# Kernel tuning notes

Measured on AMD Instinct MI355X. Metric: run time of the kernel, lower is better.

The kernel has to match this reference:

```python
import jax, jax.numpy as jnp
import numpy as np

DIM = 256
RADIUS = 3
DIAM = 2 * RADIUS + 1          # 7
NNEIGH = DIAM * DIAM           # 49
B, H, W = 2, 64, 64
EPS_LN = 1e-6
EPS_NORM = 1e-7


def conv1x1(x, w, b):
    # x: [B,Cin,H,W], w: [Cout,Cin], b: [Cout]
    return jnp.einsum('oi,bihw->bohw', w, x) + b[None, :, None, None]


def layernorm2d(x, g, b):
    # channel-wise norm as in LayerNorm2d (mean/var over channel dim)
    u = x.mean(1, keepdims=True)
    s = ((x - u) ** 2).mean(1, keepdims=True)
    xn = (x - u) / jnp.sqrt(s + EPS_LN)
    return g[None, :, None, None] * xn + b[None, :, None, None]


def unfold_reflect(x, r):
    # torch F.unfold(pad(x, reflect, r), kernel=2r+1).reshape(B,C,D*D,H,W)
    d = 2 * r + 1
    hh, ww = x.shape[2], x.shape[3]
    xp = jnp.pad(x, ((0, 0), (0, 0), (r, r), (r, r)), mode='reflect')
    pats = [xp[:, :, i:i + hh, j:j + ww] for i in range(d) for j in range(d)]
    return jnp.stack(pats, axis=2)  # [B,C,D*D,H,W]


def setup_inputs() -> dict:
    key = jax.random.key(0)
    ks = jax.random.split(key, 20)
    sc_c = 1.0 / np.sqrt(DIM)
    sc_f = 1.0 / np.sqrt(NNEIGH + DIM)
    inp = {
        'spatial_feats': jax.random.normal(ks[0], (B, DIM, H, W), jnp.float32),
        'semantic_feats': jax.random.normal(ks[1], (B, DIM, H, W), jnp.float32),
        # range_proj: conv1x1 -> LN2d -> SiLU -> conv1x1
        'rp_w1': jax.random.normal(ks[2], (DIM, DIM), jnp.float32) * sc_c,
        'rp_b1': jnp.zeros((DIM,), jnp.float32),
        'rp_g': jnp.ones((DIM,), jnp.float32),
        'rp_be': jnp.zeros((DIM,), jnp.float32),
        'rp_w2': jax.random.normal(ks[3], (DIM, DIM), jnp.float32) * sc_c,
        'rp_b2': jnp.zeros((DIM,), jnp.float32),
        # fixup_proj: conv1x1(49+C->49) -> LN2d -> SiLU -> conv1x1(49->49)
        'fp_w1': jax.random.normal(ks[4], (NNEIGH, NNEIGH + DIM), jnp.float32) * sc_f,
        'fp_b1': jnp.zeros((NNEIGH,), jnp.float32),
        'fp_g': jnp.ones((NNEIGH,), jnp.float32),
        'fp_be': jnp.zeros((NNEIGH,), jnp.float32),
        'fp_w2': jax.random.normal(ks[5], (NNEIGH, NNEIGH), jnp.float32) * (1.0 / np.sqrt(NNEIGH)),
        'fp_b2': jnp.zeros((NNEIGH,), jnp.float32),
        # output_proj: conv1x1 -> LN2d -> conv1x1
        'op_w1': jax.random.normal(ks[6], (DIM, DIM), jnp.float32) * sc_c,
        'op_b1': jnp.zeros((DIM,), jnp.float32),
        'op_g': jnp.ones((DIM,), jnp.float32),
        'op_be': jnp.zeros((DIM,), jnp.float32),
        'op_w2': jax.random.normal(ks[7], (DIM, DIM), jnp.float32) * sc_c,
        'op_b2': jnp.zeros((DIM,), jnp.float32),
        'sigma_spatial': jnp.ones((), jnp.float32),
    }
    return inp


def reference(spatial_feats, semantic_feats,
              rp_w1, rp_b1, rp_g, rp_be, rp_w2, rp_b2,
              fp_w1, fp_b1, fp_g, fp_be, fp_w2, fp_b2,
              op_w1, op_b1, op_g, op_be, op_w2, op_b2,
              sigma_spatial):
    scale = jnp.asarray(DIM ** 0.5, spatial_feats.dtype)
    # range_proj(semantic_feats)
    px = conv1x1(semantic_feats, rp_w1, rp_b1)
    px = jax.nn.silu(layernorm2d(px, rp_g, rp_be))
    px = conv1x1(px, rp_w2, rp_b2)  # [B,C,H,W]

    # spatial (Gaussian) kernel over the window
    lin = jnp.linspace(-1.0, 1.0, DIAM)
    xg, yg = jnp.meshgrid(lin, lin, indexing='ij')
    spatial_kernel = jnp.exp(-(xg ** 2 + yg ** 2) / (2.0 * sigma_spatial ** 2))
    spatial_kernel = spatial_kernel.reshape(1, NNEIGH, 1, 1)

    # range kernel: local similarity + softmax over the 49 neighbors
    queries = unfold_reflect(px, RADIUS)                       # [B,C,N,H,W]
    sim = jnp.einsum('bcnhw,bchw->bnhw', queries, px) / scale
    range_kernel = jax.nn.softmax(sim.astype(jnp.float32), axis=1).astype(px.dtype)

    # neighborhoods of spatial features
    neighborhoods = unfold_reflect(spatial_feats, RADIUS)      # [B,C,N,H,W]

    # gated fixup correction
    ck = range_kernel * spatial_kernel                          # [B,N,H,W]
    fx = conv1x1(jnp.concatenate([ck, semantic_feats], axis=1), fp_w1, fp_b1)
    fx = jax.nn.silu(layernorm2d(fx, fp_g, fp_be))
    fx = conv1x1(fx, fp_w2, fp_b2)
    ck = ck + ck * jax.nn.sigmoid(fx)
    ck = ck / (ck.sum(1, keepdims=True) + EPS_NORM)

    # weighted neighborhood sum
    out = jnp.einsum('bcnhw,bnhw->bchw', neighborhoods, ck)

    # output_proj (note: no SiLU here, matching the module)
    out = conv1x1(out, op_w1, op_b1)
    out = layernorm2d(out, op_g, op_be)
    out = conv1x1(out, op_w2, op_b2)
    return out
```

## Files before the change

### kernel.cpp

```cpp
#include <hip/hip_runtime.h>
#include <cstdint>

#define HW 4096
#define C_ 256
#define NN 49
#define KW 305

typedef __bf16 bf16;
typedef bf16 bf16x8 __attribute__((ext_vector_type(8)));
typedef bf16 bf16x4 __attribute__((ext_vector_type(4)));
typedef bf16 bf16x2 __attribute__((ext_vector_type(2)));
typedef float f32x4 __attribute__((ext_vector_type(4)));

#define GLD16(src, dst) __builtin_amdgcn_global_load_lds( \
    (const __attribute__((address_space(1))) uint32_t*)(src), \
    (__attribute__((address_space(3))) uint32_t*)(dst), 16, 0, 0)

__device__ __forceinline__ int refl(int i) { return i < 0 ? -i : (i > 63 ? 126 - i : i); }
__device__ __forceinline__ float sigmoidf_(float x) { return 1.f / (1.f + __expf(-x)); }

__global__ __launch_bounds__(256) void setup_k(const float* __restrict__ spatial,
                                               const float* __restrict__ semantic,
                                               const float* __restrict__ rp_w1,
                                               const float* __restrict__ rp_w2,
                                               const float* __restrict__ op_w1,
                                               const float* __restrict__ op_w2,
                                               const float* __restrict__ fp_w1,
                                               const float* __restrict__ fp_w2,
                                               const float* __restrict__ sigma,
                                               bf16* __restrict__ spb, bf16* __restrict__ seb,
                                               bf16* __restrict__ wrp1, bf16* __restrict__ wrp2,
                                               bf16* __restrict__ wop1, bf16* __restrict__ wop2,
                                               bf16* __restrict__ w1ckb, bf16* __restrict__ w1sb,
                                               bf16* __restrict__ w2Tg, float* __restrict__ sk)
{
    __shared__ float tile[32][33];
    const int bid = blockIdx.x, t = threadIdx.x;
    if (bid < 4096) {
        int z = bid >> 10, r = bid & 1023;
        int b = z & 1;
        const float* src = (z >> 1) ? semantic : spatial;
        bf16* dst = (z >> 1) ? seb : spb;
        int p0 = (r & 127) * 32, c0 = (r >> 7) * 32;
        int tx = t & 31, ty = t >> 5;
        const float* s = src + (size_t)b * C_ * HW;
        #pragma unroll
        for (int i = 0; i < 32; i += 8)
            tile[ty + i][tx] = s[(size_t)(c0 + ty + i) * HW + p0 + tx];
        __syncthreads();
        int p = t >> 3, cq = (t & 7) * 4;
        bf16x4 o = {(bf16)tile[cq][p], (bf16)tile[cq + 1][p], (bf16)tile[cq + 2][p], (bf16)tile[cq + 3][p]};
        *(bf16x4*)&dst[((size_t)b * HW + p0 + p) * C_ + c0 + cq] = o;
        return;
    }
    int pid = bid - 4096;
    if (pid < 256) {
        const float* src = (pid < 64) ? rp_w1 : (pid < 128) ? rp_w2 : (pid < 192) ? op_w1 : op_w2;
        bf16* dst = (pid < 64) ? wrp1 : (pid < 128) ? wrp2 : (pid < 192) ? wop1 : wop2;
        int i = ((pid & 63) * 256 + t) * 4;
        f32x4 v = *(const f32x4*)&src[i];
        bf16x4 o = {(bf16)v[0], (bf16)v[1], (bf16)v[2], (bf16)v[3]};
        *(bf16x4*)&dst[i] = o;
    } else if (pid == 256) {
        if (t < NN) {
            int i = t / 7, j = t % 7;
            float xg = (i - 3) * (1.f / 3.f), yg = (j - 3) * (1.f / 3.f);
            float s = sigma[0];
            sk[t] = __expf(-(xg * xg + yg * yg) / (2.f * s * s));
        }
    } else if (pid < 270) {
        int idx = (pid - 257) * 256 + t;
        if (idx < NN * 64) {
            int k = idx >> 6, o = idx & 63;
            w1ckb[idx] = (o < NN) ? (bf16)fp_w1[o * KW + k] : (bf16)0.f;
        }
    } else if (pid < 334) {
        int idx = (pid - 270) * 256 + t;
        int o = idx >> 8, c = idx & 255;
        w1sb[idx] = (o < NN) ? (bf16)fp_w1[o * KW + NN + c] : (bf16)0.f;
    } else {
        int idx = (pid - 334) * 256 + t;
        if (idx < NN * 64) {
            int k = idx >> 6, o = idx & 63;
            w2Tg[idx] = (o < NN) ? (bf16)fp_w2[o * NN + k] : (bf16)0.f;
        }
    }
}

__device__ __forceinline__ void stage_b(const bf16* __restrict__ Wp, bf16* dst, int kc, int t)
{
    const bf16* gB = Wp + (size_t)(t >> 2) * C_ + kc + (((t & 3) ^ ((t >> 3) & 3)) * 8);
    #pragma unroll
    for (int ii = 0; ii < 4; ++ii)
        GLD16(gB + (size_t)ii * 64 * C_, dst + ii * 2048 + t * 8);
}

template<bool SILU, int MODE>
__global__ __launch_bounds__(256) void conv_pair(const bf16* __restrict__ X,
                                                 const bf16* __restrict__ W1,
                                                 const float* __restrict__ b1v,
                                                 const float* __restrict__ g,
                                                 const float* __restrict__ be,
                                                 const bf16* __restrict__ W2,
                                                 const float* __restrict__ b2v,
                                                 void* __restrict__ Yv)
{
    __shared__ __align__(16) bf16 Xf[32 * 256];
    __shared__ __align__(16) bf16 Mid[32 * 256];
    __shared__ __align__(16) bf16 Bs[2][256 * 32];
    __shared__ float lnred[32][4][2];
    const int t = threadIdx.x;
    const int lane = t & 63, wc = t >> 6;
    const int l15 = lane & 15, kb = lane >> 4;
    const long q0 = (long)blockIdx.x * 32;

    {
        const int r8 = t >> 5, slot = t & 31;
        const bf16* gX = X + (q0 + r8) * C_ + ((slot ^ (r8 & 7)) * 8);
        #pragma unroll
        for (int i = 0; i < 4; ++i)
            GLD16(gX + (size_t)i * 8 * C_, &Xf[i * 2048 + t * 8]);
    }
    stage_b(W1, &Bs[0][0], 0, t);

    const int x7 = l15 & 7;
    const int bsl = (kb ^ ((l15 >> 1) & 3)) * 8;
    int boff[4];
    #pragma unroll
    for (int n = 0; n < 4; ++n)
        boff[n] = (wc * 64 + n * 16 + l15) * 32 + bsl;
    const int a0base = l15 * 256;
    const int a1base = (16 + l15) * 256;

    f32x4 acc[2][4];
    #pragma unroll
    for (int m = 0; m < 2; ++m)
        #pragma unroll
        for (int n = 0; n < 4; ++n) acc[m][n] = (f32x4){0.f, 0.f, 0.f, 0.f};

    __syncthreads();
    int cur = 0;
    #pragma unroll
    for (int ks = 0; ks < 8; ++ks) {
        if (ks < 7) stage_b(W1, &Bs[cur ^ 1][0], (ks + 1) * 32, t);
        const int ko = ((ks * 4 + kb) ^ x7) * 8;
        bf16x8 a0 = *(const bf16x8*)&Xf[a0base + ko];
        bf16x8 a1 = *(const bf16x8*)&Xf[a1base + ko];
        #pragma unroll
        for (int n = 0; n < 4; ++n) {
            bf16x8 b = *(const bf16x8*)&Bs[cur][boff[n]];
            acc[0][n] = __builtin_amdgcn_mfma_f32_16x16x32_bf16(a0, b, acc[0][n], 0, 0, 0);
            acc[1][n] = __builtin_amdgcn_mfma_f32_16x16x32_bf16(a1, b, acc[1][n], 0, 0, 0);
        }
        __syncthreads();
        cur ^= 1;
    }

    stage_b(W2, &Bs[0][0], 0, t);

    float s4[2][4], ss4[2][4];
    #pragma unroll
    for (int m = 0; m < 2; ++m)
        #pragma unroll
        for (int r = 0; r < 4; ++r) { s4[m][r] = 0.f; ss4[m][r] = 0.f; }
    #pragma unroll
    for (int n = 0; n < 4; ++n) {
        float bo = b1v[wc * 64 + n * 16 + l15];
        #pragma unroll
        for (int m = 0; m < 2; ++m)
            #pragma unroll
            for (int r = 0; r < 4; ++r) {
                float v = acc[m][n][r] + bo;
                acc[m][n][r] = v;
                s4[m][r] += v; ss4[m][r] += v * v;
            }
    }
    #pragma unroll
    for (int off = 1; off <= 8; off <<= 1)
        #pragma unroll
        for (int m = 0; m < 2; ++m)
            #pragma unroll
            for (int r = 0; r < 4; ++r) {
                s4[m][r]  += __shfl_xor(s4[m][r], off, 64);
                ss4[m][r] += __shfl_xor(ss4[m][r], off, 64);
            }
    if (l15 == 0) {
        #pragma unroll
        for (int m = 0; m < 2; ++m)
            #pragma unroll
            for (int r = 0; r < 4; ++r) {
                lnred[m * 16 + kb * 4 + r][wc][0] = s4[m][r];
                lnred[m * 16 + kb * 4 + r][wc][1] = ss4[m][r];
            }
    }
    __syncthreads();
    float mean[2][4], rstd[2][4];
    #pragma unroll
    for (int m = 0; m < 2; ++m)
        #pragma unroll
        for (int r = 0; r < 4; ++r) {
            int p = m * 16 + kb * 4 + r;
            float st  = lnred[p][0][0] + lnred[p][1][0] + lnred[p][2][0] + lnred[p][3][0];
            float sst = lnred[p][0][1] + lnred[p][1][1] + lnred[p][2][1] + lnred[p][3][1];
            mean[m][r] = st * (1.f / 256.f);
            float var = sst * (1.f / 256.f) - mean[m][r] * mean[m][r];
            rstd[m][r] = rsqrtf(var + 1e-6f);
        }
    #pragma unroll
    for (int n = 0; n < 4; ++n) {
        int ch = wc * 64 + n * 16 + l15;
        float gv = g[ch], bev = be[ch];
        #pragma unroll
        for (int m = 0; m < 2; ++m)
            #pragma unroll
            for (int r = 0; r < 4; ++r) {
                float y = (acc[m][n][r] - mean[m][r]) * rstd[m][r] * gv + bev;
                if (SILU) y *= sigmoidf_(y);
                int p = m * 16 + kb * 4 + r;
                Mid[p * 256 + (((ch >> 3) ^ (p & 7)) * 8) + (ch & 7)] = (bf16)y;
            }
    }
    __syncthreads();

    f32x4 acc2[2][4];
    #pragma unroll
    for (int m = 0; m < 2; ++m)
        #pragma unroll
        for (int n = 0; n < 4; ++n) acc2[m][n] = (f32x4){0.f, 0.f, 0.f, 0.f};
    cur = 0;
    #pragma unroll
    for (int ks = 0; ks < 8; ++ks) {
        if (ks < 7) stage_b(W2, &Bs[cur ^ 1][0], (ks + 1) * 32, t);
        const int ko = ((ks * 4 + kb) ^ x7) * 8;
        bf16x8 a0 = *(const bf16x8*)&Mid[a0base + ko];
        bf16x8 a1 = *(const bf16x8*)&Mid[a1base + ko];
        #pragma unroll
        for (int n = 0; n < 4; ++n) {
            bf16x8 b = *(const bf16x8*)&Bs[cur][boff[n]];
            acc2[0][n] = __builtin_amdgcn_mfma_f32_16x16x32_bf16(a0, b, acc2[0][n], 0, 0, 0);
            acc2[1][n] = __builtin_amdgcn_mfma_f32_16x16x32_bf16(a1, b, acc2[1][n], 0, 0, 0);
        }
        __syncthreads();
        cur ^= 1;
    }

    if constexpr (MODE == 0) {
        #pragma unroll
        for (int n = 0; n < 4; ++n) {
            int ch = wc * 64 + n * 16 + l15;
            float bo = b2v[ch];
            #pragma unroll
            for (int m = 0; m < 2; ++m)
                #pragma unroll
                for (int r = 0; r < 4; ++r)
                    Xf[(m * 16 + kb * 4 + r) * 256 + ch] = (bf16)(acc2[m][n][r] + bo);
        }
        __syncthreads();
        bf16* Y = (bf16*)Yv;
        const int p = t >> 3, cb = (t & 7) * 32;
        #pragma unroll
        for (int i = 0; i < 4; ++i) {
            bf16x8 v = *(const bf16x8*)&Xf[p * 256 + cb + i * 8];
            *(bf16x8*)&Y[(q0 + p) * C_ + cb + i * 8] = v;
        }
    } else {
        float* Y = (float*)Yv;
        const int bb = (int)(q0 >> 12);
        #pragma unroll
        for (int n = 0; n < 4; ++n) {
            int ch = wc * 64 + n * 16 + l15;
            float bo = b2v[ch];
            #pragma unroll
            for (int m = 0; m < 2; ++m) {
                int pp = (int)(q0 & 4095) + m * 16 + kb * 4;
                f32x4 val = {acc2[m][n][0] + bo, acc2[m][n][1] + bo,
                             acc2[m][n][2] + bo, acc2[m][n][3] + bo};
                *(f32x4*)&Y[((size_t)bb * C_ + ch) * HW + pp] = val;
            }
        }
    }
}

__global__ __launch_bounds__(256) void attn_k(const bf16* __restrict__ px,
                                              const bf16* __restrict__ spb,
                                              const bf16* __restrict__ seb,
                                              const bf16* __restrict__ w1sb,
                                              const bf16* __restrict__ w1ckb,
                                              const bf16* __restrict__ w2Tg,
                                              const float* __restrict__ b1,
                                              const float* __restrict__ b2,
                                              const float* __restrict__ g,
                                              const float* __restrict__ be,
                                              const float* __restrict__ sk,
                                              bf16* __restrict__ outb)
{
    __shared__ __align__(16) bf16 uni[100 * 128];
    __shared__ float S[112 * 17];
    __shared__ float fxs[64 * 17];
    __shared__ float ckl[16][65];
    __shared__ float hb[4][64];

    const int t = threadIdx.x, lane = t & 63, wid = t >> 6;
    const int l15 = lane & 15, kb = lane >> 4;
    const int blk = blockIdx.x;
    const int batch = blk >> 8, tt = blk & 255;
    const int h0 = (tt >> 4) * 4, w0 = (tt & 15) * 4;
    const long base = (long)batch * HW;

    const float bo  = (lane < NN) ? b1[lane] : 0.f;
    const float gl  = (lane < NN) ? g[lane] : 0.f;
    const float bel = (lane < NN) ? be[lane] : 0.f;
    const float b2l = (lane < NN) ? b2[lane] : 0.f;
    const float skv = (lane < NN) ? sk[lane] : 0.f;
    const int nn_ = (lane < NN) ? lane : 0;
    const int dy = nn_ / 7, dx = nn_ % 7;

    long sgrow;
    int sdst;
    {
        int st = t;
        (void)st;
    }
#define STAGE_UNI(ci) do { \
    _Pragma("unroll") \
    for (int i_ = 0; i_ < 7; ++i_) { \
        int st_ = i_ * 256 + t; \
        if (st_ < 1600) { \
            int u_ = st_ >> 4, s_ = st_ & 15; \
            int uy_ = (u_ * 205) >> 11, ux_ = u_ - uy_ * 10; \
            long grow_ = base + refl(h0 + uy_ - 3) * 64 + refl(w0 + ux_ - 3); \
            GLD16(spb + grow_ * C_ + (ci) * 128 + ((s_ ^ (u_ & 7)) * 8), &uni[u_ * 128 + s_ * 8]); \
        } \
    } \
} while (0)

    STAGE_UNI(0);

    const int ppy = l15 >> 2, ppx = l15 & 3;
    const long qB = base + (h0 + ppy) * 64 + (w0 + ppx);
    const bf16* bpxp = px + qB * C_ + kb * 8;
    const bf16* bsemp = seb + qB * C_ + kb * 8;

    bool valid[3], ispx[3];
    const bf16* arow[3];
    #pragma unroll
    for (int j = 0; j < 3; ++j) {
        int tid = wid + 4 * j;
        valid[j] = tid < 11;
        ispx[j] = tid < 7;
        int u = tid * 16 + l15;
        int uy = (u * 205) >> 11, ux = u - uy * 10;
        long grow = (u < 100) ? base + refl(h0 + uy - 3) * 64 + refl(w0 + ux - 3) : base;
        int o = ((tid - 7) & 3) * 16 + l15;
        arow[j] = ispx[j] ? (px + grow * C_ + kb * 8)
                          : (w1sb + (size_t)o * C_ + kb * 8);
    }

    f32x4 acc[3];
    #pragma unroll
    for (int j = 0; j < 3; ++j) acc[j] = (f32x4){0.f, 0.f, 0.f, 0.f};

    #pragma unroll
    for (int ks = 0; ks < 8; ++ks) {
        bf16x8 bp = *(const bf16x8*)(bpxp + ks * 32);
        bf16x8 bs = *(const bf16x8*)(bsemp + ks * 32);
        #pragma unroll
        for (int j = 0; j < 3; ++j) {
            if (valid[j]) {
                bf16x8 a = *(const bf16x8*)(arow[j] + ks * 32);
                acc[j] = __builtin_amdgcn_mfma_f32_16x16x32_bf16(a, ispx[j] ? bp : bs, acc[j], 0, 0, 0);
            }
        }
    }

    float w1r[NN], w2r[NN];
    #pragma unroll
    for (int k = 0; k < NN; ++k) {
        w1r[k] = (float)w1ckb[k * 64 + lane];
        w2r[k] = (float)w2Tg[k * 64 + lane];
    }

    #pragma unroll
    for (int j = 0; j < 3; ++j) {
        if (valid[j]) {
            int tid = wid + 4 * j;
            float* dst = ispx[j] ? &S[(tid * 16 + kb * 4) * 17 + l15]
                                 : &fxs[(((tid - 7) * 16) + kb * 4) * 17 + l15];
            dst[0] = acc[j][0]; dst[17] = acc[j][1]; dst[34] = acc[j][2]; dst[51] = acc[j][3];
        }
    }
    __syncthreads();

    #pragma unroll
    for (int j = 0; j < 4; ++j) {
        int p = wid * 4 + j, py = p >> 2, px4 = p & 3;
        int u = (py + dy) * 10 + px4 + dx;
        float sval = (lane < NN) ? S[u * 17 + p] * 0.0625f : -1e30f;
        float mx = sval;
        #pragma unroll
        for (int off = 32; off; off >>= 1) mx = fmaxf(mx, __shfl_xor(mx, off, 64));
        float ev = (lane < NN) ? __expf(sval - mx) : 0.f;
        float ssum = ev;
        #pragma unroll
        for (int off = 32; off; off >>= 1) ssum += __shfl_xor(ssum, off, 64);
        ckl[p][lane] = (lane < NN) ? (ev / ssum) * skv : 0.f;
    }

    #pragma unroll
    for (int j = 0; j < 4; ++j) {
        int p = wid * 4 + j;
        float fxa = 0.f, fxb = 0.f;
        #pragma unroll
        for (int k = 0; k < 48; k += 2) {
            fxa += w1r[k] * ckl[p][k];
            fxb += w1r[k + 1] * ckl[p][k + 1];
        }
        fxa += w1r[48] * ckl[p][48];
        float fx = fxs[lane * 17 + p] + bo + fxa + fxb;
        float s = fx, ss = fx * fx;
        #pragma unroll
        for (int off = 32; off; off >>= 1) {
            s  += __shfl_xor(s, off, 64);
            ss += __shfl_xor(ss, off, 64);
        }
        float mean = s * (1.f / 49.f);
        float var  = ss * (1.f / 49.f) - mean * mean;
        float rstd = rsqrtf(var + 1e-6f);
        float hv = 0.f;
        if (lane < NN) {
            float xn = (fx - mean) * rstd * gl + bel;
            hv = xn * sigmoidf_(xn);
        }
        hb[wid][lane] = hv;
        float ckv = 0.f;
        if (lane < NN) {
            float ca = 0.f, cb = 0.f;
            #pragma unroll
            for (int k = 0; k < 48; k += 2) {
                ca += w2r[k] * hb[wid][k];
                cb += w2r[k + 1] * hb[wid][k + 1];
            }
            ca += w2r[48] * hb[wid][48];
            ckv = ckl[p][lane] * (1.f + sigmoidf_(b2l + ca + cb));
        }
        float tot = ckv;
        #pragma unroll
        for (int off = 32; off; off >>= 1) tot += __shfl_xor(tot, off, 64);
        ckl[p][lane] = (lane < NN) ? ckv / (tot + 1e-7f) : 0.f;
    }
    __syncthreads();

    const int sub = lane >> 4;
    const int p = wid * 4 + sub;
    const int py = p >> 2, px4 = p & 3;
    const long q = base + (h0 + py) * 64 + (w0 + px4);
    const int ub = py * 10 + px4;

    #pragma unroll
    for (int ci = 0; ci < 2; ++ci) {
        if (ci == 1) {
            __syncthreads();
            STAGE_UNI(1);
            __syncthreads();
        }
        float a[8];
        #pragma unroll
        for (int e = 0; e < 8; ++e) a[e] = 0.f;
        for (int dyy = 0; dyy < 7; ++dyy) {
            bf16x8 v[7];
            #pragma unroll
            for (int dxx = 0; dxx < 7; ++dxx) {
                int u = ub + dyy * 10 + dxx;
                v[dxx] = *(const bf16x8*)&uni[u * 128 + ((l15 ^ (u & 7)) * 8)];
            }
            #pragma unroll
            for (int dxx = 0; dxx < 7; ++dxx) {
                float cv = ckl[p][dyy * 7 + dxx];
                #pragma unroll
                for (int e = 0; e < 8; ++e) a[e] += cv * (float)v[dxx][e];
            }
        }
        bf16x8 ov;
        #pragma unroll
        for (int e = 0; e < 8; ++e) ov[e] = (bf16)a[e];
        *(bf16x8*)&outb[q * C_ + ci * 128 + l15 * 8] = ov;
    }
#undef STAGE_UNI
}

extern "C" void kernel_launch(void* const* d_in, const int* in_sizes, int n_in,
                              void* d_out, int out_size, void* d_ws, size_t ws_size,
                              hipStream_t stream)
{
    const float* spatial  = (const float*)d_in[0];
    const float* semantic = (const float*)d_in[1];
    const float* rp_w1 = (const float*)d_in[2];
    const float* rp_b1 = (const float*)d_in[3];
    const float* rp_g  = (const float*)d_in[4];
    const float* rp_be = (const float*)d_in[5];
    const float* rp_w2 = (const float*)d_in[6];
    const float* rp_b2 = (const float*)d_in[7];
    const float* fp_w1 = (const float*)d_in[8];
    const float* fp_b1 = (const float*)d_in[9];
    const float* fp_g  = (const float*)d_in[10];
    const float* fp_be = (const float*)d_in[11];
    const float* fp_w2 = (const float*)d_in[12];
    const float* fp_b2 = (const float*)d_in[13];
    const float* op_w1 = (const float*)d_in[14];
    const float* op_b1 = (const float*)d_in[15];
    const float* op_g  = (const float*)d_in[16];
    const float* op_be = (const float*)d_in[17];
    const float* op_w2 = (const float*)d_in[18];
    const float* op_b2 = (const float*)d_in[19];
    const float* sigma = (const float*)d_in[20];

    const size_t NPX = 2 * (size_t)HW;
    float* ws = (float*)d_ws;
    float* sk    = ws;
    bf16* bfbase = (bf16*)(sk + 64);
    bf16* spb = bfbase;
    bf16* seb = spb + NPX * C_;
    bf16* t0  = seb + NPX * C_;
    bf16* t1  = t0  + NPX * C_;
    bf16* wrp1 = t1 + NPX * C_;
    bf16* wrp2 = wrp1 + C_ * C_;
    bf16* wop1 = wrp2 + C_ * C_;
    bf16* wop2 = wop1 + C_ * C_;
    bf16* w1sb = wop2 + C_ * C_;
    bf16* w2Tg = w1sb + 64 * C_;
    bf16* w1ckb = w2Tg + 3200;

    setup_k<<<4443, 256, 0, stream>>>(spatial, semantic, rp_w1, rp_w2, op_w1, op_w2,
                                      fp_w1, fp_w2, sigma,
                                      spb, seb, wrp1, wrp2, wop1, wop2,
                                      w1ckb, w1sb, w2Tg, sk);

    conv_pair<true, 0><<<256, 256, 0, stream>>>(seb, wrp1, rp_b1, rp_g, rp_be, wrp2, rp_b2, t1);

    attn_k<<<512, 256, 0, stream>>>(t1, spb, seb, w1sb, w1ckb, w2Tg, fp_b1, fp_b2,
                                    fp_g, fp_be, sk, t0);

    conv_pair<false, 1><<<256, 256, 0, stream>>>(t0, wop1, op_b1, op_g, op_be, wop2, op_b2, d_out);
}
```

Measured before the change: 66.02 us.

## Fuse output projection (conv-LN-conv) into attention kernel epilogue

The per-pixel output_proj (two 1x1 convs with LayerNorm between) is computed inside the attention kernel on its 16-pixel tile using MFMA, instead of writing a bf16 intermediate and launching a separate conv_pair kernel. Shared memory is repurposed through a single byte arena to hold the tile, a mid buffer and double-buffered weight slices. This removes one launch and the round trip of the intermediate through global memory. In exchange, each block restreams both full 256x256 weight matrices for only 16 pixels, which is low reuse, and the larger shared-memory footprint may reduce occupancy.

```diff
diff --git a/kernel.cpp b/kernel.cpp
--- a/kernel.cpp
+++ b/kernel.cpp
@@ -9,7 +9,6 @@
 typedef __bf16 bf16;
 typedef bf16 bf16x8 __attribute__((ext_vector_type(8)));
 typedef bf16 bf16x4 __attribute__((ext_vector_type(4)));
-typedef bf16 bf16x2 __attribute__((ext_vector_type(2)));
 typedef float f32x4 __attribute__((ext_vector_type(4)));
 
 #define GLD16(src, dst) __builtin_amdgcn_global_load_lds( \
@@ -281,24 +280,36 @@
     }
 }
 
-__global__ __launch_bounds__(256) void attn_k(const bf16* __restrict__ px,
-                                              const bf16* __restrict__ spb,
-                                              const bf16* __restrict__ seb,
-                                              const bf16* __restrict__ w1sb,
-                                              const bf16* __restrict__ w1ckb,
-                                              const bf16* __restrict__ w2Tg,
-                                              const float* __restrict__ b1,
-                                              const float* __restrict__ b2,
-                                              const float* __restrict__ g,
-                                              const float* __restrict__ be,
-                                              const float* __restrict__ sk,
-                                              bf16* __restrict__ outb)
+__global__ __launch_bounds__(256) void attn_out_k(const bf16* __restrict__ px,
+                                                  const bf16* __restrict__ spb,
+                                                  const bf16* __restrict__ seb,
+                                                  const bf16* __restrict__ w1sb,
+                                                  const bf16* __restrict__ w1ckb,
+                                                  const bf16* __restrict__ w2Tg,
+                                                  const float* __restrict__ b1,
+                                                  const float* __restrict__ b2,
+                                                  const float* __restrict__ g,
+                                                  const float* __restrict__ be,
+                                                  const float* __restrict__ sk,
+                                                  const bf16* __restrict__ wop1,
+                                                  const float* __restrict__ ob1,
+                                                  const float* __restrict__ og,
+                                                  const float* __restrict__ obe,
+                                                  const bf16* __restrict__ wop2,
+                                                  const float* __restrict__ ob2,
+                                                  float* __restrict__ Y)
 {
-    __shared__ __align__(16) bf16 uni[100 * 128];
-    __shared__ float S[112 * 17];
-    __shared__ float fxs[64 * 17];
-    __shared__ float ckl[16][65];
-    __shared__ float hb[4][64];
+    __shared__ __align__(16) char shm[49664];
+    bf16*  uni = (bf16*)(shm);
+    float* ckl = (float*)(shm + 25600);
+    float* hb  = (float*)(shm + 29760);
+    float* S   = (float*)(shm + 32768);
+    float* fxs = (float*)(shm + 40384);
+    bf16*  Xg  = (bf16*)(shm + 32768);
+    bf16*  Mid = (bf16*)(shm + 40960);
+    bf16*  Bs0 = (bf16*)(shm);
+    bf16*  Bs1 = (bf16*)(shm + 16384);
+    float* lnred = (float*)(shm + 49152);
 
     const int t = threadIdx.x, lane = t & 63, wid = t >> 6;
     const int l15 = lane & 15, kb = lane >> 4;
@@ -315,12 +326,6 @@
     const int nn_ = (lane < NN) ? lane : 0;
     const int dy = nn_ / 7, dx = nn_ % 7;
 
-    long sgrow;
-    int sdst;
-    {
-        int st = t;
-        (void)st;
-    }
 #define STAGE_UNI(ci) do { \
     _Pragma("unroll") \
     for (int i_ = 0; i_ < 7; ++i_) { \
@@ -403,7 +408,7 @@
         float ssum = ev;
         #pragma unroll
         for (int off = 32; off; off >>= 1) ssum += __shfl_xor(ssum, off, 64);
-        ckl[p][lane] = (lane < NN) ? (ev / ssum) * skv : 0.f;
+        ckl[p * 65 + lane] = (lane < NN) ? (ev / ssum) * skv : 0.f;
     }
 
     #pragma unroll
@@ -412,10 +417,10 @@
         float fxa = 0.f, fxb = 0.f;
         #pragma unroll
         for (int k = 0; k < 48; k += 2) {
-            fxa += w1r[k] * ckl[p][k];
-            fxb += w1r[k + 1] * ckl[p][k + 1];
-        }
-        fxa += w1r[48] * ckl[p][48];
+            fxa += w1r[k] * ckl[p * 65 + k];
+            fxb += w1r[k + 1] * ckl[p * 65 + k + 1];
+        }
+        fxa += w1r[48] * ckl[p * 65 + 48];
         float fx = fxs[lane * 17 + p] + bo + fxa + fxb;
         float s = fx, ss = fx * fx;
         #pragma unroll
@@ -431,30 +436,27 @@
             float xn = (fx - mean) * rstd * gl + bel;
             hv = xn * sigmoidf_(xn);
         }
-        hb[wid][lane] = hv;
+        hb[wid * 64 + lane] = hv;
         float ckv = 0.f;
         if (lane < NN) {
             float ca = 0.f, cb = 0.f;
             #pragma unroll
             for (int k = 0; k < 48; k += 2) {
-                ca += w2r[k] * hb[wid][k];
-                cb += w2r[k + 1] * hb[wid][k + 1];
-            }
-            ca += w2r[48] * hb[wid][48];
-            ckv = ckl[p][lane] * (1.f + sigmoidf_(b2l + ca + cb));
+                ca += w2r[k] * hb[wid * 64 + k];
+                cb += w2r[k + 1] * hb[wid * 64 + k + 1];
+            }
+            ca += w2r[48] * hb[wid * 64 + 48];
+            ckv = ckl[p * 65 + lane] * (1.f + sigmoidf_(b2l + ca + cb));
         }
         float tot = ckv;
         #pragma unroll
         for (int off = 32; off; off >>= 1) tot += __shfl_xor(tot, off, 64);
-        ckl[p][lane] = (lane < NN) ? ckv / (tot + 1e-7f) : 0.f;
+        ckl[p * 65 + lane] = (lane < NN) ? ckv / (tot + 1e-7f) : 0.f;
     }
     __syncthreads();
 
     const int sub = lane >> 4;
-    const int p = wid * 4 + sub;
-    const int py = p >> 2, px4 = p & 3;
-    const long q = base + (h0 + py) * 64 + (w0 + px4);
-    const int ub = py * 10 + px4;
+    const int gp = wid * 4 + sub;
 
     #pragma unroll
     for (int ci = 0; ci < 2; ++ci) {
@@ -463,6 +465,7 @@
             STAGE_UNI(1);
             __syncthreads();
         }
+        const int ub = (gp >> 2) * 10 + (gp & 3);
         float a[8];
         #pragma unroll
         for (int e = 0; e < 8; ++e) a[e] = 0.f;
@@ -475,7 +478,7 @@
             }
             #pragma unroll
             for (int dxx = 0; dxx < 7; ++dxx) {
-                float cv = ckl[p][dyy * 7 + dxx];
+                float cv = ckl[gp * 65 + dyy * 7 + dxx];
                 #pragma unroll
                 for (int e = 0; e < 8; ++e) a[e] += cv * (float)v[dxx][e];
             }
@@ -483,7 +486,117 @@
         bf16x8 ov;
         #pragma unroll
         for (int e = 0; e < 8; ++e) ov[e] = (bf16)a[e];
-        *(bf16x8*)&outb[q * C_ + ci * 128 + l15 * 8] = ov;
+        *(bf16x8*)&Xg[gp * 256 + (((ci * 16 + l15) ^ (gp & 7)) * 8)] = ov;
+    }
+    __syncthreads();
+
+    stage_b(wop1, Bs0, 0, t);
+
+    const int x7 = l15 & 7;
+    const int bsl = (kb ^ ((l15 >> 1) & 3)) * 8;
+    int boff[4];
+    #pragma unroll
+    for (int n = 0; n < 4; ++n)
+        boff[n] = (wid * 64 + n * 16 + l15) * 32 + bsl;
+
+    f32x4 cacc[4];
+    #pragma unroll
+    for (int n = 0; n < 4; ++n) cacc[n] = (f32x4){0.f, 0.f, 0.f, 0.f};
+
+    __syncthreads();
+    int cur = 0;
+    #pragma unroll
+    for (int ks = 0; ks < 8; ++ks) {
+        if (ks < 7) stage_b(wop1, cur ? Bs0 : Bs1, (ks + 1) * 32, t);
+        const int ko = ((ks * 4 + kb) ^ x7) * 8;
+        bf16x8 a = *(const bf16x8*)&Xg[l15 * 256 + ko];
+        #pragma unroll
+        for (int n = 0; n < 4; ++n) {
+            bf16x8 b = *(const bf16x8*)&((cur ? Bs1 : Bs0)[boff[n]]);
+            cacc[n] = __builtin_amdgcn_mfma_f32_16x16x32_bf16(a, b, cacc[n], 0, 0, 0);
+        }
+        __syncthreads();
+        cur ^= 1;
+    }
+
+    stage_b(wop2, Bs0, 0, t);
+
+    float s4[4] = {0.f, 0.f, 0.f, 0.f}, ss4[4] = {0.f, 0.f, 0.f, 0.f};
+    #pragma unroll
+    for (int n = 0; n < 4; ++n) {
+        float bv = ob1[wid * 64 + n * 16 + l15];
+        #pragma unroll
+        for (int r = 0; r < 4; ++r) {
+            float v = cacc[n][r] + bv;
+            cacc[n][r] = v;
+            s4[r] += v; ss4[r] += v * v;
+        }
+    }
+    #pragma unroll
+    for (int off = 1; off <= 8; off <<= 1)
+        #pragma unroll
+        for (int r = 0; r < 4; ++r) {
+            s4[r]  += __shfl_xor(s4[r], off, 64);
+            ss4[r] += __shfl_xor(ss4[r], off, 64);
+        }
+    if (l15 == 0) {
+        #pragma unroll
+        for (int r = 0; r < 4; ++r) {
+            lnred[((kb * 4 + r) * 4 + wid) * 2 + 0] = s4[r];
+            lnred[((kb * 4 + r) * 4 + wid) * 2 + 1] = ss4[r];
+        }
+    }
+    __syncthreads();
+    float mean[4], rstd[4];
+    #pragma unroll
+    for (int r = 0; r < 4; ++r) {
+        int p = kb * 4 + r;
+        float st  = lnred[(p * 4 + 0) * 2] + lnred[(p * 4 + 1) * 2] + lnred[(p * 4 + 2) * 2] + lnred[(p * 4 + 3) * 2];
+        float sst = lnred[(p * 4 + 0) * 2 + 1] + lnred[(p * 4 + 1) * 2 + 1] + lnred[(p * 4 + 2) * 2 + 1] + lnred[(p * 4 + 3) * 2 + 1];
+        mean[r] = st * (1.f / 256.f);
+        float var = sst * (1.f / 256.f) - mean[r] * mean[r];
+        rstd[r] = rsqrtf(var + 1e-6f);
+    }
+    #pragma unroll
+    for (int n = 0; n < 4; ++n) {
+        int ch = wid * 64 + n * 16 + l15;
+        float gv = og[ch], bev = obe[ch];
+        #pragma unroll
+        for (int r = 0; r < 4; ++r) {
+            float y = (cacc[n][r] - mean[r]) * rstd[r] * gv + bev;
+            int p = kb * 4 + r;
+            Mid[p * 256 + (((ch >> 3) ^ (p & 7)) * 8) + (ch & 7)] = (bf16)y;
+        }
+    }
+    __syncthreads();
+
+    f32x4 cacc2[4];
+    #pragma unroll
+    for (int n = 0; n < 4; ++n) cacc2[n] = (f32x4){0.f, 0.f, 0.f, 0.f};
+    cur = 0;
+    #pragma unroll
+    for (int ks = 0; ks < 8; ++ks) {
+        if (ks < 7) stage_b(wop2, cur ? Bs0 : Bs1, (ks + 1) * 32, t);
+        const int ko = ((ks * 4 + kb) ^ x7) * 8;
+        bf16x8 a = *(const bf16x8*)&Mid[l15 * 256 + ko];
+        #pragma unroll
+        for (int n = 0; n < 4; ++n) {
+            bf16x8 b = *(const bf16x8*)&((cur ? Bs1 : Bs0)[boff[n]]);
+            cacc2[n] = __builtin_amdgcn_mfma_f32_16x16x32_bf16(a, b, cacc2[n], 0, 0, 0);
+        }
+        __syncthreads();
+        cur ^= 1;
+    }
+
+    {
+        const size_t rowbase = ((size_t)batch * C_) * HW + (size_t)(h0 + kb) * 64 + w0;
+        #pragma unroll
+        for (int n = 0; n < 4; ++n) {
+            int ch = wid * 64 + n * 16 + l15;
+            float bv = ob2[ch];
+            f32x4 val = {cacc2[n][0] + bv, cacc2[n][1] + bv, cacc2[n][2] + bv, cacc2[n][3] + bv};
+            *(f32x4*)&Y[rowbase + (size_t)ch * HW] = val;
+        }
     }
 #undef STAGE_UNI
 }
@@ -520,8 +633,7 @@
     bf16* bfbase = (bf16*)(sk + 64);
     bf16* spb = bfbase;
     bf16* seb = spb + NPX * C_;
-    bf16* t0  = seb + NPX * C_;
-    bf16* t1  = t0  + NPX * C_;
+    bf16* t1  = seb + NPX * C_;
     bf16* wrp1 = t1 + NPX * C_;
     bf16* wrp2 = wrp1 + C_ * C_;
     bf16* wop1 = wrp2 + C_ * C_;
@@ -537,8 +649,8 @@
 
     conv_pair<true, 0><<<256, 256, 0, stream>>>(seb, wrp1, rp_b1, rp_g, rp_be, wrp2, rp_b2, t1);
 
-    attn_k<<<512, 256, 0, stream>>>(t1, spb, seb, w1sb, w1ckb, w2Tg, fp_b1, fp_b2,
-                                    fp_g, fp_be, sk, t0);
-
-    conv_pair<false, 1><<<256, 256, 0, stream>>>(t0, wop1, op_b1, op_g, op_be, wop2, op_b2, d_out);
+    attn_out_k<<<512, 256, 0, stream>>>(t1, spb, seb, w1sb, w1ckb, w2Tg, fp_b1, fp_b2,
+                                        fp_g, fp_be, sk,
+                                        wop1, op_b1, op_g, op_be, wop2, op_b2,
+                                        (float*)d_out);
 }
```

Measured after the change: 65.74 us. Within noise of the previous version (-0.4%).
